# Optimization experiments

Hardware: AMD Instinct MI355X
Metric: run time of the kernel (lower is better)

## Reference

```python
import jax, jax.numpy as jnp
import numpy as np

TP, M, K, N_GLOBAL = 8, 4096, 8192, 8192
K_LOCAL = K // TP      # 1024
N_LOCAL = N_GLOBAL // TP  # 1024


def setup_inputs() -> dict:
    key = jax.random.key(0)
    k1, k2, k3 = jax.random.split(key, 3)
    # all_act[r] is rank r's local activation shard (M, K_local);
    # the fused kernel all-gathers these into the gathered buffer.
    all_act = jax.random.normal(k1, (TP, M, K_LOCAL), dtype=jnp.float32)
    # local_W: this rank's weight shard, full K rows, N_local columns.
    local_W = jax.random.normal(k2, (K, N_LOCAL), dtype=jnp.float32) / np.sqrt(K)
    bias = jax.random.normal(k3, (N_LOCAL,), dtype=jnp.float32)
    return {"all_act": all_act, "local_W": local_W, "bias": bias}


def reference(all_act, local_W, bias):
    # Kernel accumulates, per source rank r:
    #   acc += A_shard[r] (M, K_local) @ W[r*K_local:(r+1)*K_local] (K_local, N_local)
    # which equals A_full @ W_local with A_full the K-concat of shards.
    W_shards = local_W.reshape(TP, K_LOCAL, N_LOCAL)
    out = jnp.einsum('rmk,rkn->mn', all_act, W_shards)  # (M, N_local)
    return out + bias[None, :]
```

## Files before the change

kernel.cpp:

```cpp
#include <hip/hip_runtime.h>
#include <stdint.h>

#define TP_      8
#define M_DIM    4096
#define K_DIM    8192
#define N_DIM    1024
#define KL_      1024
#define BM       256
#define BN       256
#define SPLITK   4
#define KSLICE   (K_DIM / SPLITK)
#define NT       (KSLICE / 64)
#define MN4      (M_DIM * N_DIM / 4)
#define KCHUNKS  (K_DIM / 32)

typedef _Float16 f16;
typedef f16 f16x8 __attribute__((ext_vector_type(8)));
typedef float f32x4 __attribute__((ext_vector_type(4)));

__device__ __forceinline__ f16x8 cvt8(float4 a, float4 b) {
    f16x8 r;
    r[0] = (f16)a.x; r[1] = (f16)a.y; r[2] = (f16)a.z; r[3] = (f16)a.w;
    r[4] = (f16)b.x; r[5] = (f16)b.y; r[6] = (f16)b.z; r[7] = (f16)b.w;
    return r;
}

__device__ __forceinline__ void lds_load16(const void* g, void* l) {
    __builtin_amdgcn_global_load_lds(
        (const __attribute__((address_space(1))) void*)g,
        (__attribute__((address_space(3))) void*)l, 16, 0, 0);
}


__global__ __launch_bounds__(256) void conv_a_kernel(
        const float* __restrict__ act, f16* __restrict__ Afrag) {
    const int t = threadIdx.x;
    const int chunkId = blockIdx.x * 4 + (t >> 6);
    const int lane = t & 63;
    const int q  = lane >> 4;
    const int rr = lane & 15;
    const int mg  = chunkId >> 8;
    const int k32 = chunkId & 255;
    const int k  = k32 * 32 + q * 8;
    const int r  = k >> 10;
    const int kl = k & (KL_ - 1);
    const int m  = mg * 16 + rr;
    const float4* src = (const float4*)(act + ((size_t)r * M_DIM + m) * KL_ + kl);
    float4 a = src[0], b = src[1];
    *(f16x8*)(Afrag + (size_t)chunkId * 512 + lane * 8) = cvt8(a, b);
}

__global__ __launch_bounds__(256) void conv_w_kernel(
        const float* __restrict__ W, f16* __restrict__ Bfrag) {
    __shared__ float tile[64][68];
    const int t  = threadIdx.x;
    const int n0 = blockIdx.x * 64;
    const int k0 = blockIdx.y * 64;
    #pragma unroll
    for (int l = 0; l < 4; l++) {
        int kr = l * 16 + (t >> 4);
        float4 v = *(const float4*)&W[(size_t)(k0 + kr) * N_DIM + n0 + (t & 15) * 4];
        *(float4*)&tile[kr][(t & 15) * 4] = v;
    }
    __syncthreads();
    const int jtl   = t >> 6;
    const int kt32l = (t >> 5) & 1;
    const int u     = t & 31;
    const int rr    = u & 15;
    const int qp    = u >> 4;
    f16x8 h0, h1;
    #pragma unroll
    for (int kk = 0; kk < 8; kk++)
        h0[kk] = (f16)tile[kt32l * 32 + qp * 16 + kk][jtl * 16 + rr];
    #pragma unroll
    for (int kk = 0; kk < 8; kk++)
        h1[kk] = (f16)tile[kt32l * 32 + qp * 16 + 8 + kk][jtl * 16 + rr];
    size_t chunk = (size_t)(n0 / 16 + jtl) * KCHUNKS + (k0 / 32 + kt32l);
    f16* dst = Bfrag + chunk * 512;
    *(f16x8*)(dst + ((2 * qp)     * 16 + rr) * 8) = h0;
    *(f16x8*)(dst + ((2 * qp + 1) * 16 + rr) * 8) = h1;
}

__global__ __launch_bounds__(512, 2) void gemm_frag_kernel(
        const f16* __restrict__ Afrag,
        const f16* __restrict__ Bfrag,
        float* __restrict__ part) {
    __shared__ f16 sm[2][64 * 512];

    const int tid  = threadIdx.x;
    const int w    = tid >> 6;
    const int lane = tid & 63;
    const int q    = lane >> 4;
    const int rr   = lane & 15;
    const int wr   = w >> 2;
    const int wc   = w & 3;

    const int id   = blockIdx.x;
    const int xcd  = id & 7;
    const int slot = id >> 3;
    const int z    = xcd >> 1;
    const int mb   = (slot >> 2) * 2 + (xcd & 1);
    const int nb   = slot & 3;
    const int row0 = mb * BM;
    const int col0 = nb * BN;
    const int kb32 = z * (KSLICE / 32);
    const int mg0  = row0 >> 4;
    const int ng0  = col0 >> 4;

    f32x4 acc[8][4];
    #pragma unroll
    for (int m = 0; m < 8; m++)
        #pragma unroll
        for (int n = 0; n < 4; n++)
            acc[m][n] = (f32x4){0.f, 0.f, 0.f, 0.f};

    f16x8 af[8];
    f16x8 bf[2];

#define STAGE_A(B_, T_, K2_) do { \
    const int kt32_ = kb32 + 2 * (T_) + (K2_); \
    _Pragma("unroll") \
    for (int j_ = 0; j_ < 2; j_++) { \
        const int mg_ = 2 * w + j_; \
        const f16* g_ = Afrag + ((size_t)(mg0 + mg_) * KCHUNKS + kt32_) * 512 + lane * 8; \
        lds_load16(g_, &sm[B_][(mg_ * 2 + (K2_)) * 512 + lane * 8]); \
    } \
} while (0)

#define STAGE_B(B_, T_, K2_) do { \
    const int kt32_ = kb32 + 2 * (T_) + (K2_); \
    _Pragma("unroll") \
    for (int j_ = 0; j_ < 2; j_++) { \
        const int ng_ = 2 * w + j_; \
        const f16* g_ = Bfrag + ((size_t)(ng0 + ng_) * KCHUNKS + kt32_) * 512 + lane * 8; \
        lds_load16(g_, &sm[B_][(32 + ng_ * 2 + (K2_)) * 512 + lane * 8]); \
    } \
} while (0)

#define READ_A(B_, K2_) do { \
    _Pragma("unroll") \
    for (int mi_ = 0; mi_ < 8; mi_++) \
        af[mi_] = *(const f16x8*)&sm[B_][((wr * 8 + mi_) * 2 + (K2_)) * 512 + lane * 8]; \
} while (0)

#define READ_B(B_, K2_, NH_) do { \
    _Pragma("unroll") \
    for (int ni_ = 0; ni_ < 2; ni_++) \
        bf[ni_] = *(const f16x8*)&sm[B_][(32 + (wc * 4 + (NH_) * 2 + ni_) * 2 + (K2_)) * 512 + lane * 8]; \
} while (0)

#define MFMA16(NH_) do { \
    __builtin_amdgcn_s_setprio(1); \
    _Pragma("unroll") \
    for (int mi_ = 0; mi_ < 8; mi_++) \
        _Pragma("unroll") \
        for (int ni_ = 0; ni_ < 2; ni_++) \
            acc[mi_][(NH_) * 2 + ni_] = __builtin_amdgcn_mfma_f32_16x16x32_f16( \
                af[mi_], bf[ni_], acc[mi_][(NH_) * 2 + ni_], 0, 0, 0); \
    __builtin_amdgcn_s_setprio(0); \
} while (0)

#define BAR() do { \
    asm volatile("" ::: "memory"); \
    __builtin_amdgcn_s_barrier(); \
    asm volatile("" ::: "memory"); \
} while (0)
#define SBAR0() __builtin_amdgcn_sched_barrier(0)
#define VM4() asm volatile("s_waitcnt vmcnt(4)" ::: "memory")
#define VM0() asm volatile("s_waitcnt vmcnt(0)" ::: "memory")

#define TILE(P_, T_, STG_, VMMID_, VMEND_) do { \
    READ_A(P_, 0); READ_B(P_, 0, 0); \
    if (STG_) STAGE_A((P_) ^ 1, (T_) + 1, 0); \
    BAR(); SBAR0(); MFMA16(0); BAR(); \
    READ_B(P_, 0, 1); \
    if (STG_) STAGE_B((P_) ^ 1, (T_) + 1, 0); \
    BAR(); SBAR0(); MFMA16(1); VMMID_; BAR(); \
    READ_A(P_, 1); READ_B(P_, 1, 0); \
    if (STG_) STAGE_A((P_) ^ 1, (T_) + 1, 1); \
    BAR(); SBAR0(); MFMA16(0); BAR(); \
    READ_B(P_, 1, 1); \
    if (STG_) STAGE_B((P_) ^ 1, (T_) + 1, 1); \
    BAR(); SBAR0(); MFMA16(1); VMEND_; BAR(); \
} while (0)

    STAGE_A(0, 0, 0);
    STAGE_B(0, 0, 0);
    STAGE_A(0, 0, 1);
    STAGE_B(0, 0, 1);
    VM4();
    BAR();

    #pragma unroll 1
    for (int t = 0; t < 30; t += 2) {
        TILE(0, t,     1, VM4(), VM4());
        TILE(1, t + 1, 1, VM4(), VM4());
    }
    TILE(0, 30, 1, VM4(), VM4());
    TILE(1, 31, 0, VM0(), (void)0);

    float* Pz = part + (size_t)z * M_DIM * N_DIM;
    #pragma unroll
    for (int m = 0; m < 8; m++) {
        const int gm = row0 + wr * 128 + m * 16 + q * 4;
        #pragma unroll
        for (int n = 0; n < 4; n++) {
            const int gn = col0 + wc * 64 + n * 16 + rr;
            #pragma unroll
            for (int r2 = 0; r2 < 4; r2++)
                Pz[(size_t)(gm + r2) * N_DIM + gn] = acc[m][n][r2];
        }
    }
#undef STAGE_A
#undef STAGE_B
#undef READ_A
#undef READ_B
#undef MFMA16
#undef BAR
#undef SBAR0
#undef VM4
#undef VM0
#undef TILE
}

__global__ __launch_bounds__(256) void reduce_kernel(
        const float* __restrict__ part, const float* __restrict__ bias,
        float* __restrict__ out) {
    int p = blockIdx.x * 256 + threadIdx.x;
    const float4* P = (const float4*)part;
    float4 s0 = P[p];
    float4 s1 = P[p + MN4];
    float4 s2 = P[p + 2 * MN4];
    float4 s3 = P[p + 3 * MN4];
    float4 b  = ((const float4*)bias)[p & (N_DIM / 4 - 1)];
    float4 r;
    r.x = s0.x + s1.x + s2.x + s3.x + b.x;
    r.y = s0.y + s1.y + s2.y + s3.y + b.y;
    r.z = s0.z + s1.z + s2.z + s3.z + b.z;
    r.w = s0.w + s1.w + s2.w + s3.w + b.w;
    ((float4*)out)[p] = r;
}

__global__ void gemm_fallback_kernel(const float* __restrict__ act,
                                     const float* __restrict__ W,
                                     const float* __restrict__ bias,
                                     float* __restrict__ out) {
    __shared__ float sA2[32][33];
    __shared__ float sB2[32][33];
    int tx = threadIdx.x, ty = threadIdx.y;
    int m = blockIdx.y * 32 + ty;
    int n = blockIdx.x * 32 + tx;
    float acc = 0.f;
    for (int kt = 0; kt < K_DIM; kt += 32) {
        int ka = kt + tx;
        int r = ka >> 10, kl = ka & (KL_ - 1);
        sA2[ty][tx] = act[((size_t)r * M_DIM + m) * KL_ + kl];
        sB2[ty][tx] = W[(size_t)(kt + ty) * N_DIM + n];
        __syncthreads();
        #pragma unroll
        for (int kk = 0; kk < 32; kk++) acc += sA2[ty][kk] * sB2[kk][tx];
        __syncthreads();
    }
    out[(size_t)m * N_DIM + n] = acc + bias[n];
}

extern "C" void kernel_launch(void* const* d_in, const int* in_sizes, int n_in,
                              void* d_out, int out_size, void* d_ws, size_t ws_size,
                              hipStream_t stream) {
    const float* all_act = (const float*)d_in[0];
    const float* local_W = (const float*)d_in[1];
    const float* bias    = (const float*)d_in[2];
    float* out = (float*)d_out;

    const size_t partBytes = (size_t)SPLITK * M_DIM * N_DIM * sizeof(float);
    const size_t elemsA    = (size_t)M_DIM * K_DIM;
    const size_t elemsW    = (size_t)K_DIM * N_DIM;
    const size_t need = partBytes + elemsA * sizeof(f16) + elemsW * sizeof(f16);

    if (ws_size < need) {
        gemm_fallback_kernel<<<dim3(N_DIM / 32, M_DIM / 32), dim3(32, 32), 0, stream>>>(
            all_act, local_W, bias, out);
        return;
    }

    float* part  = (float*)d_ws;
    f16*   Afrag = (f16*)((char*)d_ws + partBytes);
    f16*   Bfrag = Afrag + elemsA;

    conv_a_kernel<<<(M_DIM / 16) * (K_DIM / 32) / 4, 256, 0, stream>>>(all_act, Afrag);
    conv_w_kernel<<<dim3(N_DIM / 64, K_DIM / 64), 256, 0, stream>>>(local_W, Bfrag);
    gemm_frag_kernel<<<256, 512, 0, stream>>>(Afrag, Bfrag, part);
    reduce_kernel<<<MN4 / 256, 256, 0, stream>>>(part, bias, out);
}
```

Before: 301.3 us.

## Fuse fp32-to-fp16 activation conversion into the GEMM main loop

```diff
diff --git a/kernel.cpp b/kernel.cpp
--- a/kernel.cpp
+++ b/kernel.cpp
@@ -10,7 +10,6 @@
 #define BN       256
 #define SPLITK   4
 #define KSLICE   (K_DIM / SPLITK)
-#define NT       (KSLICE / 64)
 #define MN4      (M_DIM * N_DIM / 4)
 #define KCHUNKS  (K_DIM / 32)
 
@@ -31,24 +30,6 @@
         (__attribute__((address_space(3))) void*)l, 16, 0, 0);
 }
 
-
-__global__ __launch_bounds__(256) void conv_a_kernel(
-        const float* __restrict__ act, f16* __restrict__ Afrag) {
-    const int t = threadIdx.x;
-    const int chunkId = blockIdx.x * 4 + (t >> 6);
-    const int lane = t & 63;
-    const int q  = lane >> 4;
-    const int rr = lane & 15;
-    const int mg  = chunkId >> 8;
-    const int k32 = chunkId & 255;
-    const int k  = k32 * 32 + q * 8;
-    const int r  = k >> 10;
-    const int kl = k & (KL_ - 1);
-    const int m  = mg * 16 + rr;
-    const float4* src = (const float4*)(act + ((size_t)r * M_DIM + m) * KL_ + kl);
-    float4 a = src[0], b = src[1];
-    *(f16x8*)(Afrag + (size_t)chunkId * 512 + lane * 8) = cvt8(a, b);
-}
 
 __global__ __launch_bounds__(256) void conv_w_kernel(
         const float* __restrict__ W, f16* __restrict__ Bfrag) {
@@ -81,8 +62,8 @@
     *(f16x8*)(dst + ((2 * qp + 1) * 16 + rr) * 8) = h1;
 }
 
-__global__ __launch_bounds__(512, 2) void gemm_frag_kernel(
-        const f16* __restrict__ Afrag,
+__global__ __launch_bounds__(512, 2) void gemm_fused_kernel(
+        const float* __restrict__ act,
         const f16* __restrict__ Bfrag,
         float* __restrict__ part) {
     __shared__ f16 sm[2][64 * 512];
@@ -94,6 +75,8 @@
     const int rr   = lane & 15;
     const int wr   = w >> 2;
     const int wc   = w & 3;
+    const int rt   = tid >> 1;
+    const int hh   = tid & 1;
 
     const int id   = blockIdx.x;
     const int xcd  = id & 7;
@@ -103,9 +86,11 @@
     const int nb   = slot & 3;
     const int row0 = mb * BM;
     const int col0 = nb * BN;
-    const int kb32 = z * (KSLICE / 32);
-    const int mg0  = row0 >> 4;
+    const int kb   = z * KSLICE;
+    const int kb32 = kb >> 5;
     const int ng0  = col0 >> 4;
+
+    const size_t aRow = (size_t)(row0 + rt) * KL_ + hh * 16;
 
     f32x4 acc[8][4];
     #pragma unroll
@@ -116,14 +101,27 @@
 
     f16x8 af[8];
     f16x8 bf[2];
-
-#define STAGE_A(B_, T_, K2_) do { \
-    const int kt32_ = kb32 + 2 * (T_) + (K2_); \
-    _Pragma("unroll") \
-    for (int j_ = 0; j_ < 2; j_++) { \
-        const int mg_ = 2 * w + j_; \
-        const f16* g_ = Afrag + ((size_t)(mg0 + mg_) * KCHUNKS + kt32_) * 512 + lane * 8; \
-        lds_load16(g_, &sm[B_][(mg_ * 2 + (K2_)) * 512 + lane * 8]); \
+    float4 aa[8];
+
+#define LOADA(T_) do { \
+    _Pragma("unroll") \
+    for (int k2_ = 0; k2_ < 2; k2_++) { \
+        const int k_ = kb + (T_) * 64 + k2_ * 32; \
+        const float* ap_ = act + (size_t)(k_ >> 10) * ((size_t)M_DIM * KL_) \
+                           + aRow + (k_ & (KL_ - 1)); \
+        _Pragma("unroll") \
+        for (int i_ = 0; i_ < 4; i_++) aa[k2_ * 4 + i_] = ((const float4*)ap_)[i_]; \
+    } \
+} while (0)
+
+#define CVTWA(B_) do { \
+    _Pragma("unroll") \
+    for (int k2_ = 0; k2_ < 2; k2_++) { \
+        f16x8 u0_ = cvt8(aa[k2_ * 4 + 0], aa[k2_ * 4 + 1]); \
+        f16x8 u1_ = cvt8(aa[k2_ * 4 + 2], aa[k2_ * 4 + 3]); \
+        f16* dA_ = &sm[B_][(((rt >> 4) * 2) + k2_) * 512]; \
+        *(f16x8*)(dA_ + ((2 * hh)     * 16 + (rt & 15)) * 8) = u0_; \
+        *(f16x8*)(dA_ + ((2 * hh + 1) * 16 + (rt & 15)) * 8) = u1_; \
     } \
 } while (0)
 
@@ -166,37 +164,41 @@
     asm volatile("" ::: "memory"); \
 } while (0)
 #define SBAR0() __builtin_amdgcn_sched_barrier(0)
-#define VM4() asm volatile("s_waitcnt vmcnt(4)" ::: "memory")
-#define VM0() asm volatile("s_waitcnt vmcnt(0)" ::: "memory")
+#define VM0()  asm volatile("s_waitcnt vmcnt(0)" ::: "memory")
+#define VM2()  asm volatile("s_waitcnt vmcnt(2)" ::: "memory")
+#define VM10() asm volatile("s_waitcnt vmcnt(10)" ::: "memory")
+#define LGK0() asm volatile("s_waitcnt lgkmcnt(0)" ::: "memory")
 
 #define TILE(P_, T_, STG_, VMMID_, VMEND_) do { \
+    if (STG_) LOADA((T_) + 1); \
     READ_A(P_, 0); READ_B(P_, 0, 0); \
-    if (STG_) STAGE_A((P_) ^ 1, (T_) + 1, 0); \
     BAR(); SBAR0(); MFMA16(0); BAR(); \
     READ_B(P_, 0, 1); \
     if (STG_) STAGE_B((P_) ^ 1, (T_) + 1, 0); \
     BAR(); SBAR0(); MFMA16(1); VMMID_; BAR(); \
+    if (STG_) CVTWA((P_) ^ 1); \
     READ_A(P_, 1); READ_B(P_, 1, 0); \
-    if (STG_) STAGE_A((P_) ^ 1, (T_) + 1, 1); \
     BAR(); SBAR0(); MFMA16(0); BAR(); \
     READ_B(P_, 1, 1); \
     if (STG_) STAGE_B((P_) ^ 1, (T_) + 1, 1); \
     BAR(); SBAR0(); MFMA16(1); VMEND_; BAR(); \
 } while (0)
 
-    STAGE_A(0, 0, 0);
+    LOADA(0);
     STAGE_B(0, 0, 0);
-    STAGE_A(0, 0, 1);
     STAGE_B(0, 0, 1);
-    VM4();
-    BAR();
+    CVTWA(0);
+    VM0();
+    LGK0();
+    __builtin_amdgcn_s_barrier();
+    asm volatile("" ::: "memory");
 
     #pragma unroll 1
     for (int t = 0; t < 30; t += 2) {
-        TILE(0, t,     1, VM4(), VM4());
-        TILE(1, t + 1, 1, VM4(), VM4());
-    }
-    TILE(0, 30, 1, VM4(), VM4());
+        TILE(0, t,     1, VM10(), VM2());
+        TILE(1, t + 1, 1, VM10(), VM2());
+    }
+    TILE(0, 30, 1, VM10(), VM2());
     TILE(1, 31, 0, VM0(), (void)0);
 
     float* Pz = part + (size_t)z * M_DIM * N_DIM;
@@ -211,15 +213,18 @@
                 Pz[(size_t)(gm + r2) * N_DIM + gn] = acc[m][n][r2];
         }
     }
-#undef STAGE_A
+#undef LOADA
+#undef CVTWA
 #undef STAGE_B
 #undef READ_A
 #undef READ_B
 #undef MFMA16
 #undef BAR
 #undef SBAR0
-#undef VM4
 #undef VM0
+#undef VM2
+#undef VM10
+#undef LGK0
 #undef TILE
 }
 
@@ -273,9 +278,8 @@
     float* out = (float*)d_out;
 
     const size_t partBytes = (size_t)SPLITK * M_DIM * N_DIM * sizeof(float);
-    const size_t elemsA    = (size_t)M_DIM * K_DIM;
     const size_t elemsW    = (size_t)K_DIM * N_DIM;
-    const size_t need = partBytes + elemsA * sizeof(f16) + elemsW * sizeof(f16);
+    const size_t need = partBytes + elemsW * sizeof(f16);
 
     if (ws_size < need) {
         gemm_fallback_kernel<<<dim3(N_DIM / 32, M_DIM / 32), dim3(32, 32), 0, stream>>>(
@@ -284,11 +288,9 @@
     }
 
     float* part  = (float*)d_ws;
-    f16*   Afrag = (f16*)((char*)d_ws + partBytes);
-    f16*   Bfrag = Afrag + elemsA;
-
-    conv_a_kernel<<<(M_DIM / 16) * (K_DIM / 32) / 4, 256, 0, stream>>>(all_act, Afrag);
+    f16*   Bfrag = (f16*)((char*)d_ws + partBytes);
+
     conv_w_kernel<<<dim3(N_DIM / 64, K_DIM / 64), 256, 0, stream>>>(local_W, Bfrag);
-    gemm_frag_kernel<<<256, 512, 0, stream>>>(Afrag, Bfrag, part);
+    gemm_fused_kernel<<<256, 512, 0, stream>>>(all_act, Bfrag, part);
     reduce_kernel<<<MN4 / 256, 256, 0, stream>>>(part, bias, out);
 }
```

New measurement: 308.3 us. 2.3% more time.
